# Kernel tuning notes

Hardware: AMD Instinct MI355X
Metric: run time of the kernel (lower is better)

Reference implementation:

```python
import jax, jax.numpy as jnp
import numpy as np
import math

S, B, E, H = 4096, 2, 1024, 16
D = E // H  # 64, projection dim used for scaling
LN_EPS = 1e-5

def setup_inputs() -> dict:
    key = jax.random.key(0)
    ks = jax.random.split(key, 3)
    std = 1.0 / math.sqrt(E)
    return {
        "src_emb": jax.random.normal(ks[0], (S, B, E), dtype=jnp.float32),
        "gamma": jnp.ones((E,), dtype=jnp.float32),
        "beta": jnp.zeros((E,), dtype=jnp.float32),
        "Wq": jax.random.normal(ks[1], (E, D), dtype=jnp.float32) * std,
        "bq": jnp.zeros((D,), dtype=jnp.float32),
        "Wk": jax.random.normal(ks[2], (E, D), dtype=jnp.float32) * std,
        "bk": jnp.zeros((D,), dtype=jnp.float32),
    }

def reference(src_emb, gamma, beta, Wq, bq, Wk, bk):
    # [S, B, E] -> [B, S, E]
    x = jnp.swapaxes(src_emb, 0, 1)
    # LayerNorm over last dim
    mu = jnp.mean(x, axis=-1, keepdims=True)
    var = jnp.mean(jnp.square(x - mu), axis=-1, keepdims=True)
    x = (x - mu) * jax.lax.rsqrt(var + LN_EPS) * gamma + beta
    # Q/K projections to head dim D
    q = x @ Wq + bq  # [B, S, D]
    k = x @ Wk + bk  # [B, S, D]
    scale = 1.0 / math.sqrt(D)
    # scaled bmm: [B, S(t), S(s)]
    scores = jnp.einsum("btd,bsd->bts", q * scale, k)
    # unnormalized softmax: row-max subtract then exp
    scores = scores - jnp.max(scores, axis=-1, keepdims=True)
    return jnp.exp(scores)
```

## Files before the change

kernel.cpp:

```cpp
#include <hip/hip_runtime.h>
#include <math.h>


typedef __attribute__((ext_vector_type(4))) float f32x4;
typedef __attribute__((ext_vector_type(8))) short bf16x8;
typedef __attribute__((ext_vector_type(8))) unsigned short u16x8;

#define SLEN 4096
#define BATCH 2
#define EDIM 1024
#define DDIM 64
#define KCH 256
#define XS_STRIDE 260
#define QK_STRIDE 136

__device__ __forceinline__ unsigned short f2bf(float f) {
    unsigned int u = __float_as_uint(f);
    u += 0x7FFFu + ((u >> 16) & 1u);
    return (unsigned short)(u >> 16);
}
__device__ __forceinline__ float bf2f(unsigned short h) {
    return __uint_as_float(((unsigned int)h) << 16);
}

__global__ __launch_bounds__(256) void wprep_kernel(
    const float* __restrict__ Wq, const float* __restrict__ Wk,
    unsigned short* __restrict__ whf, unsigned short* __restrict__ wlf)
{
    const int slot = blockIdx.x * 256 + threadIdx.x;
    const int ct = slot >> 11;
    const int kg = (slot >> 6) & 31;
    const int l  = slot & 63;
    const int c  = ct * 16 + (l & 15);
    const int kb = kg * 32 + ((l >> 4) & 3) * 8;
    const float* Wm = (c < DDIM) ? (Wq + c) : (Wk + (c - DDIM));
    u16x8 hv, lv;
#pragma unroll
    for (int j = 0; j < 8; ++j) {
        const float v = Wm[(size_t)(kb + j) * DDIM];
        const unsigned short h = f2bf(v);
        hv[j] = h;
        lv[j] = f2bf(v - bf2f(h));
    }
    *reinterpret_cast<u16x8*>(whf + (size_t)slot * 8) = hv;
    *reinterpret_cast<u16x8*>(wlf + (size_t)slot * 8) = lv;
}

__global__ __launch_bounds__(256, 2) void ln_proj_kernel(
    const float* __restrict__ src, const float* __restrict__ gamma,
    const float* __restrict__ beta,
    const float* __restrict__ bq, const float* __restrict__ bk,
    const unsigned short* __restrict__ whf, const unsigned short* __restrict__ wlf,
    unsigned short* __restrict__ qhf, unsigned short* __restrict__ qlf,
    unsigned short* __restrict__ khf, unsigned short* __restrict__ klf)
{
    __shared__ float xs[2][16][XS_STRIDE];
    __shared__ float2 stats[16];
    const int tid  = threadIdx.x;
    const int lane = tid & 63;
    const int wv   = tid >> 6;
    const int bid  = blockIdx.x;
    const int b    = bid >> 8;
    const int s0   = (bid & 255) * 16;

    for (int ii = 0; ii < 4; ++ii) {
        const int i = wv * 4 + ii;
        const float* row = src + ((size_t)(s0 + i) * BATCH + b) * EDIM;
        float sum = 0.f, sq = 0.f;
#pragma unroll
        for (int k = 0; k < 4; ++k) {
            float4 v = *reinterpret_cast<const float4*>(row + k * 256 + lane * 4);
            sum += v.x + v.y + v.z + v.w;
            sq  += v.x*v.x + v.y*v.y + v.z*v.z + v.w*v.w;
        }
#pragma unroll
        for (int off = 1; off < 64; off <<= 1) {
            sum += __shfl_xor(sum, off);
            sq  += __shfl_xor(sq,  off);
        }
        if (lane == 0) {
            const float mu   = sum * (1.f / EDIM);
            const float rstd = rsqrtf(sq * (1.f / EDIM) - mu * mu + 1e-5f);
            stats[i] = make_float2(mu, rstd);
        }
    }
    __syncthreads();

    const int srow = tid >> 4;
    const int se   = (tid & 15) * 4;
    const float* srcrow = src + ((size_t)(s0 + srow) * BATCH + b) * EDIM;
    const float smu = stats[srow].x;
    const float srs = stats[srow].y;

    const int ct0 = wv * 2;
    const int arow = lane & 15;
    const int koff = (lane >> 4) * 8;
    f32x4 acc0 = {0.f, 0.f, 0.f, 0.f};
    f32x4 acc1 = {0.f, 0.f, 0.f, 0.f};

#pragma unroll
    for (int t = 0; t < 4; ++t) {
        const int e = se + t * 64;
        float4 v  = *reinterpret_cast<const float4*>(srcrow + e);
        float4 g  = *reinterpret_cast<const float4*>(gamma + e);
        float4 bt = *reinterpret_cast<const float4*>(beta + e);
        float4 o;
        o.x = (v.x - smu) * srs * g.x + bt.x;
        o.y = (v.y - smu) * srs * g.y + bt.y;
        o.z = (v.z - smu) * srs * g.z + bt.z;
        o.w = (v.w - smu) * srs * g.w + bt.w;
        *reinterpret_cast<float4*>(&xs[0][srow][e]) = o;
    }
    __syncthreads();

    for (int c = 0; c < 4; ++c) {
        const int cur = c & 1;
        if (c < 3) {
            const int k0 = (c + 1) * KCH;
#pragma unroll
            for (int t = 0; t < 4; ++t) {
                const int e = se + t * 64;
                float4 v  = *reinterpret_cast<const float4*>(srcrow + k0 + e);
                float4 g  = *reinterpret_cast<const float4*>(gamma + k0 + e);
                float4 bt = *reinterpret_cast<const float4*>(beta + k0 + e);
                float4 o;
                o.x = (v.x - smu) * srs * g.x + bt.x;
                o.y = (v.y - smu) * srs * g.y + bt.y;
                o.z = (v.z - smu) * srs * g.z + bt.z;
                o.w = (v.w - smu) * srs * g.w + bt.w;
                *reinterpret_cast<float4*>(&xs[cur ^ 1][srow][e]) = o;
            }
        }
#pragma unroll 2
        for (int ks = 0; ks < 8; ++ks) {
            const int kg = c * 8 + ks;
            const float* xp = &xs[cur][arow][ks * 32 + koff];
            const float4 v0 = *reinterpret_cast<const float4*>(xp);
            const float4 v1 = *reinterpret_cast<const float4*>(xp + 4);
            const float vv[8] = {v0.x, v0.y, v0.z, v0.w, v1.x, v1.y, v1.z, v1.w};
            bf16x8 ah, al;
#pragma unroll
            for (int j = 0; j < 8; ++j) {
                const unsigned short h = f2bf(vv[j]);
                ah[j] = (short)h;
                al[j] = (short)f2bf(vv[j] - bf2f(h));
            }
            const size_t wb0 = ((size_t)(ct0 * 32 + kg) * 64 + lane) * 8;
            const size_t wb1 = wb0 + (size_t)32 * 64 * 8;
            const bf16x8 bh0 = *reinterpret_cast<const bf16x8*>(whf + wb0);
            const bf16x8 bl0 = *reinterpret_cast<const bf16x8*>(wlf + wb0);
            const bf16x8 bh1 = *reinterpret_cast<const bf16x8*>(whf + wb1);
            const bf16x8 bl1 = *reinterpret_cast<const bf16x8*>(wlf + wb1);
            acc0 = __builtin_amdgcn_mfma_f32_16x16x32_bf16(ah, bh0, acc0, 0, 0, 0);
            acc0 = __builtin_amdgcn_mfma_f32_16x16x32_bf16(al, bh0, acc0, 0, 0, 0);
            acc0 = __builtin_amdgcn_mfma_f32_16x16x32_bf16(ah, bl0, acc0, 0, 0, 0);
            acc0 = __builtin_amdgcn_mfma_f32_16x16x32_bf16(al, bl0, acc0, 0, 0, 0);
            acc1 = __builtin_amdgcn_mfma_f32_16x16x32_bf16(ah, bh1, acc1, 0, 0, 0);
            acc1 = __builtin_amdgcn_mfma_f32_16x16x32_bf16(al, bh1, acc1, 0, 0, 0);
            acc1 = __builtin_amdgcn_mfma_f32_16x16x32_bf16(ah, bl1, acc1, 0, 0, 0);
            acc1 = __builtin_amdgcn_mfma_f32_16x16x32_bf16(al, bl1, acc1, 0, 0, 0);
        }
        __syncthreads();
    }

    float* qk = &xs[0][0][0];
    {
        const int cj0 = ct0 * 16 + (lane & 15);
        const int cj1 = cj0 + 16;
        const int r0  = (lane >> 4) * 4;
        const float bv0 = (cj0 < DDIM) ? bq[cj0] : bk[cj0 - DDIM];
        const float bv1 = (cj1 < DDIM) ? bq[cj1] : bk[cj1 - DDIM];
        const int cb0 = (cj0 < DDIM) ? cj0 : (68 + cj0 - DDIM);
        const int cb1 = (cj1 < DDIM) ? cj1 : (68 + cj1 - DDIM);
#pragma unroll
        for (int r = 0; r < 4; ++r) {
            qk[(r0 + r) * QK_STRIDE + cb0] = acc0[r] + bv0;
            qk[(r0 + r) * QK_STRIDE + cb1] = acc1[r] + bv1;
        }
    }
    __syncthreads();

    {
        const int l2  = tid & 63;
        const int dc  = (tid >> 6) & 1;
        const int isK = tid >> 7;
        const int row = l2 & 15;
        const int d0  = dc * 32 + ((l2 >> 4) & 3) * 8;
        const float* p = &qk[row * QK_STRIDE + (isK ? 68 : 0) + d0];
        const float sc = isK ? 1.0f : 0.125f;
        u16x8 hvv, lvv;
#pragma unroll
        for (int j = 0; j < 8; ++j) {
            const float vq = p[j] * sc;
            const unsigned short h = f2bf(vq);
            hvv[j] = h;
            lvv[j] = f2bf(vq - bf2f(h));
        }
        const size_t base = ((((size_t)b * 256 + (size_t)(bid & 255)) * 2 + dc) * 512) + (size_t)l2 * 8;
        *reinterpret_cast<u16x8*>((isK ? khf : qhf) + base) = hvv;
        *reinterpret_cast<u16x8*>((isK ? klf : qlf) + base) = lvv;
    }
}

__global__ __launch_bounds__(1024, 1) void score_kernel(
    const unsigned short* __restrict__ qhf, const unsigned short* __restrict__ qlf,
    const unsigned short* __restrict__ khf, const unsigned short* __restrict__ klf,
    float* __restrict__ out)
{
    __shared__ float wmax[16 * 16];
    __shared__ float fmax_s[16];
    const int tid = threadIdx.x;
    const int l   = tid & 63;
    const int w   = tid >> 6;
    const int bid = blockIdx.x;
    const int b   = bid >> 8;
    const int rt  = bid & 255;

    const size_t abase = (((size_t)b * 256 + rt) * 2) * 512 + (size_t)l * 8;
    const bf16x8 qh0 = *reinterpret_cast<const bf16x8*>(qhf + abase);
    const bf16x8 qh1 = *reinterpret_cast<const bf16x8*>(qhf + abase + 512);
    const bf16x8 ql0 = *reinterpret_cast<const bf16x8*>(qlf + abase);
    const bf16x8 ql1 = *reinterpret_cast<const bf16x8*>(qlf + abase + 512);

    f32x4 acc[16];
#pragma unroll
    for (int i = 0; i < 16; ++i) acc[i] = (f32x4){0.f, 0.f, 0.f, 0.f};

#pragma unroll
    for (int i = 0; i < 16; ++i) {
        const int ct = w * 16 + i;
        const size_t kb = (((size_t)b * 256 + ct) * 2) * 512 + (size_t)l * 8;
        const bf16x8 kh0 = *reinterpret_cast<const bf16x8*>(khf + kb);
        const bf16x8 kh1 = *reinterpret_cast<const bf16x8*>(khf + kb + 512);
        const bf16x8 kl0 = *reinterpret_cast<const bf16x8*>(klf + kb);
        const bf16x8 kl1 = *reinterpret_cast<const bf16x8*>(klf + kb + 512);
        f32x4 a = acc[i];
        a = __builtin_amdgcn_mfma_f32_16x16x32_bf16(qh0, kh0, a, 0, 0, 0);
        a = __builtin_amdgcn_mfma_f32_16x16x32_bf16(qh1, kh1, a, 0, 0, 0);
        a = __builtin_amdgcn_mfma_f32_16x16x32_bf16(qh0, kl0, a, 0, 0, 0);
        a = __builtin_amdgcn_mfma_f32_16x16x32_bf16(qh1, kl1, a, 0, 0, 0);
        a = __builtin_amdgcn_mfma_f32_16x16x32_bf16(ql0, kh0, a, 0, 0, 0);
        a = __builtin_amdgcn_mfma_f32_16x16x32_bf16(ql1, kh1, a, 0, 0, 0);
        acc[i] = a;
    }

    float m4[4];
#pragma unroll
    for (int r = 0; r < 4; ++r) {
        m4[r] = acc[0][r];
#pragma unroll
        for (int i = 1; i < 16; ++i) m4[r] = fmaxf(m4[r], acc[i][r]);
    }
#pragma unroll
    for (int off = 1; off < 16; off <<= 1) {
#pragma unroll
        for (int r = 0; r < 4; ++r) m4[r] = fmaxf(m4[r], __shfl_xor(m4[r], off));
    }
    const int rgrp = l >> 4;
    if ((l & 15) == 0) {
#pragma unroll
        for (int r = 0; r < 4; ++r) wmax[w * 16 + rgrp * 4 + r] = m4[r];
    }
    __syncthreads();
    if (tid < 16) {
        float m = wmax[tid];
#pragma unroll
        for (int ww = 1; ww < 16; ++ww) m = fmaxf(m, wmax[ww * 16 + tid]);
        fmax_s[tid] = m;
    }
    __syncthreads();

    float fm[4];
#pragma unroll
    for (int r = 0; r < 4; ++r) fm[r] = fmax_s[rgrp * 4 + r];
    const int cres = l & 15;
    const size_t obase = ((size_t)b * SLEN + (size_t)rt * 16) * SLEN;
#pragma unroll
    for (int i = 0; i < 16; ++i) {
        const int col = (w * 16 + i) * 16 + cres;
#pragma unroll
        for (int r = 0; r < 4; ++r)
            out[obase + (size_t)(rgrp * 4 + r) * SLEN + col] = __expf(acc[i][r] - fm[r]);
    }
}

extern "C" void kernel_launch(void* const* d_in, const int* in_sizes, int n_in,
                              void* d_out, int out_size, void* d_ws, size_t ws_size,
                              hipStream_t stream) {
    (void)in_sizes; (void)n_in;
    const float* src   = (const float*)d_in[0];
    const float* gamma = (const float*)d_in[1];
    const float* beta  = (const float*)d_in[2];
    const float* Wq    = (const float*)d_in[3];
    const float* bq    = (const float*)d_in[4];
    const float* Wk    = (const float*)d_in[5];
    const float* bk    = (const float*)d_in[6];
    float* out = (float*)d_out;

    unsigned short* ws  = (unsigned short*)d_ws;
    unsigned short* qhf = ws;
    unsigned short* qlf = ws + (1u << 19);
    unsigned short* khf = ws + (2u << 19);
    unsigned short* klf = ws + (3u << 19);

    const size_t wfrag_shorts = 131072;
    const size_t need_bytes = (4u << 20) + 2 * 256 * 1024;
    unsigned short *whf, *wlf;
    if (ws_size >= need_bytes) {
        whf = ws + (4u << 19);
        wlf = whf + wfrag_shorts;
    } else {
        const size_t out_bytes = (size_t)out_size * 4;
        char* tail = (char*)d_out + (out_bytes - (2 * 256 * 1024 + 4096));
        whf = (unsigned short*)tail;
        wlf = whf + wfrag_shorts;
    }

    hipLaunchKernelGGL(wprep_kernel, dim3(64), dim3(256), 0, stream,
                       Wq, Wk, whf, wlf);
    hipLaunchKernelGGL(ln_proj_kernel, dim3(512), dim3(256), 0, stream,
                       src, gamma, beta, bq, bk, whf, wlf, qhf, qlf, khf, klf);
    hipLaunchKernelGGL(score_kernel, dim3(512), dim3(1024), 0, stream,
                       qhf, qlf, khf, klf, out);
}
```

Before: 75.08 us.

## Split fused LayerNorm-projection into LN, split-K MFMA projection, and reduce kernels

Replaces the single fused LayerNorm-plus-projection kernel with three kernels. The first normalizes rows and writes bf16 hi/lo fragments to global memory. The second runs a split-K MFMA projection over 1024 blocks, each covering two row tiles and one K quarter, writing partial sums. The third reduces the partials, adds bias and packs the Q/K fragments. The aim is more parallelism and MFMA reuse of weight fragments across two row tiles, at the cost of extra launches and a global round trip for the normalized activations and partial sums.

New measurement: 84.93 us. +13.1%, slower.

```diff
diff --git a/kernel.cpp b/kernel.cpp
--- a/kernel.cpp
+++ b/kernel.cpp
@@ -10,8 +10,6 @@
 #define BATCH 2
 #define EDIM 1024
 #define DDIM 64
-#define KCH 256
-#define XS_STRIDE 260
 #define QK_STRIDE 136
 
 __device__ __forceinline__ unsigned short f2bf(float f) {
@@ -46,22 +44,18 @@
     *reinterpret_cast<u16x8*>(wlf + (size_t)slot * 8) = lv;
 }
 
-__global__ __launch_bounds__(256, 2) void ln_proj_kernel(
+__global__ __launch_bounds__(256, 2) void ln_split_kernel(
     const float* __restrict__ src, const float* __restrict__ gamma,
     const float* __restrict__ beta,
-    const float* __restrict__ bq, const float* __restrict__ bk,
-    const unsigned short* __restrict__ whf, const unsigned short* __restrict__ wlf,
-    unsigned short* __restrict__ qhf, unsigned short* __restrict__ qlf,
-    unsigned short* __restrict__ khf, unsigned short* __restrict__ klf)
-{
-    __shared__ float xs[2][16][XS_STRIDE];
+    unsigned short* __restrict__ xh, unsigned short* __restrict__ xl)
+{
     __shared__ float2 stats[16];
     const int tid  = threadIdx.x;
     const int lane = tid & 63;
     const int wv   = tid >> 6;
-    const int bid  = blockIdx.x;
-    const int b    = bid >> 8;
-    const int s0   = (bid & 255) * 16;
+    const int gt   = blockIdx.x;
+    const int b    = gt >> 8;
+    const int s0   = (gt & 255) * 16;
 
     for (int ii = 0; ii < 4; ++ii) {
         const int i = wv * 4 + ii;
@@ -86,97 +80,129 @@
     }
     __syncthreads();
 
-    const int srow = tid >> 4;
-    const int se   = (tid & 15) * 4;
-    const float* srcrow = src + ((size_t)(s0 + srow) * BATCH + b) * EDIM;
-    const float smu = stats[srow].x;
-    const float srs = stats[srow].y;
-
-    const int ct0 = wv * 2;
-    const int arow = lane & 15;
-    const int koff = (lane >> 4) * 8;
+    const int row = lane & 15;
+    const int k4  = ((lane >> 4) & 3) * 8;
+    const float* srow = src + ((size_t)(s0 + row) * BATCH + b) * EDIM;
+    const float mu   = stats[row].x;
+    const float rstd = stats[row].y;
+#pragma unroll
+    for (int i = 0; i < 8; ++i) {
+        const int kg = wv * 8 + i;
+        const int kb = kg * 32 + k4;
+        const float4 va = *reinterpret_cast<const float4*>(srow + kb);
+        const float4 vb = *reinterpret_cast<const float4*>(srow + kb + 4);
+        const float4 ga = *reinterpret_cast<const float4*>(gamma + kb);
+        const float4 gb = *reinterpret_cast<const float4*>(gamma + kb + 4);
+        const float4 ba = *reinterpret_cast<const float4*>(beta + kb);
+        const float4 bb = *reinterpret_cast<const float4*>(beta + kb + 4);
+        const float vv[8] = {
+            (va.x - mu) * rstd * ga.x + ba.x, (va.y - mu) * rstd * ga.y + ba.y,
+            (va.z - mu) * rstd * ga.z + ba.z, (va.w - mu) * rstd * ga.w + ba.w,
+            (vb.x - mu) * rstd * gb.x + bb.x, (vb.y - mu) * rstd * gb.y + bb.y,
+            (vb.z - mu) * rstd * gb.z + bb.z, (vb.w - mu) * rstd * gb.w + bb.w };
+        u16x8 hv, lv;
+#pragma unroll
+        for (int j = 0; j < 8; ++j) {
+            const unsigned short h = f2bf(vv[j]);
+            hv[j] = h;
+            lv[j] = f2bf(vv[j] - bf2f(h));
+        }
+        const size_t slot = ((size_t)gt * 32 + kg) * 64 + lane;
+        *reinterpret_cast<u16x8*>(xh + slot * 8) = hv;
+        *reinterpret_cast<u16x8*>(xl + slot * 8) = lv;
+    }
+}
+
+__global__ __launch_bounds__(512, 4) void proj_kernel(
+    const unsigned short* __restrict__ xh, const unsigned short* __restrict__ xl,
+    const unsigned short* __restrict__ whf, const unsigned short* __restrict__ wlf,
+    float* __restrict__ pc)
+{
+    __shared__ u16x8 sa[2][2][8][64];
+    const int tid  = threadIdx.x;
+    const int lane = tid & 63;
+    const int ct   = tid >> 6;
+    const int bid  = blockIdx.x;
+    const int mg   = bid >> 2;
+    const int ksl  = bid & 3;
+    const int gt0  = mg * 2;
+
+    u16x8* sl = &sa[0][0][0][0];
+#pragma unroll
+    for (int p = 0; p < 4; ++p) {
+        const int sidx = p * 512 + tid;
+        const int hl   = sidx >> 10;
+        const int rem  = sidx & 1023;
+        const int t2   = rem >> 9;
+        const int kg   = (rem >> 6) & 7;
+        const int ln   = rem & 63;
+        const size_t gslot = (((size_t)(gt0 + t2)) * 32 + ksl * 8 + kg) * 64 + ln;
+        const unsigned short* srcp = hl ? xl : xh;
+        sl[sidx] = *reinterpret_cast<const u16x8*>(srcp + gslot * 8);
+    }
+    __syncthreads();
+
     f32x4 acc0 = {0.f, 0.f, 0.f, 0.f};
     f32x4 acc1 = {0.f, 0.f, 0.f, 0.f};
-
-#pragma unroll
-    for (int t = 0; t < 4; ++t) {
-        const int e = se + t * 64;
-        float4 v  = *reinterpret_cast<const float4*>(srcrow + e);
-        float4 g  = *reinterpret_cast<const float4*>(gamma + e);
-        float4 bt = *reinterpret_cast<const float4*>(beta + e);
-        float4 o;
-        o.x = (v.x - smu) * srs * g.x + bt.x;
-        o.y = (v.y - smu) * srs * g.y + bt.y;
-        o.z = (v.z - smu) * srs * g.z + bt.z;
-        o.w = (v.w - smu) * srs * g.w + bt.w;
-        *reinterpret_cast<float4*>(&xs[0][srow][e]) = o;
-    }
-    __syncthreads();
-
-    for (int c = 0; c < 4; ++c) {
-        const int cur = c & 1;
-        if (c < 3) {
-            const int k0 = (c + 1) * KCH;
-#pragma unroll
-            for (int t = 0; t < 4; ++t) {
-                const int e = se + t * 64;
-                float4 v  = *reinterpret_cast<const float4*>(srcrow + k0 + e);
-                float4 g  = *reinterpret_cast<const float4*>(gamma + k0 + e);
-                float4 bt = *reinterpret_cast<const float4*>(beta + k0 + e);
-                float4 o;
-                o.x = (v.x - smu) * srs * g.x + bt.x;
-                o.y = (v.y - smu) * srs * g.y + bt.y;
-                o.z = (v.z - smu) * srs * g.z + bt.z;
-                o.w = (v.w - smu) * srs * g.w + bt.w;
-                *reinterpret_cast<float4*>(&xs[cur ^ 1][srow][e]) = o;
-            }
-        }
-#pragma unroll 2
-        for (int ks = 0; ks < 8; ++ks) {
-            const int kg = c * 8 + ks;
-            const float* xp = &xs[cur][arow][ks * 32 + koff];
-            const float4 v0 = *reinterpret_cast<const float4*>(xp);
-            const float4 v1 = *reinterpret_cast<const float4*>(xp + 4);
-            const float vv[8] = {v0.x, v0.y, v0.z, v0.w, v1.x, v1.y, v1.z, v1.w};
-            bf16x8 ah, al;
-#pragma unroll
-            for (int j = 0; j < 8; ++j) {
-                const unsigned short h = f2bf(vv[j]);
-                ah[j] = (short)h;
-                al[j] = (short)f2bf(vv[j] - bf2f(h));
-            }
-            const size_t wb0 = ((size_t)(ct0 * 32 + kg) * 64 + lane) * 8;
-            const size_t wb1 = wb0 + (size_t)32 * 64 * 8;
-            const bf16x8 bh0 = *reinterpret_cast<const bf16x8*>(whf + wb0);
-            const bf16x8 bl0 = *reinterpret_cast<const bf16x8*>(wlf + wb0);
-            const bf16x8 bh1 = *reinterpret_cast<const bf16x8*>(whf + wb1);
-            const bf16x8 bl1 = *reinterpret_cast<const bf16x8*>(wlf + wb1);
-            acc0 = __builtin_amdgcn_mfma_f32_16x16x32_bf16(ah, bh0, acc0, 0, 0, 0);
-            acc0 = __builtin_amdgcn_mfma_f32_16x16x32_bf16(al, bh0, acc0, 0, 0, 0);
-            acc0 = __builtin_amdgcn_mfma_f32_16x16x32_bf16(ah, bl0, acc0, 0, 0, 0);
-            acc0 = __builtin_amdgcn_mfma_f32_16x16x32_bf16(al, bl0, acc0, 0, 0, 0);
-            acc1 = __builtin_amdgcn_mfma_f32_16x16x32_bf16(ah, bh1, acc1, 0, 0, 0);
-            acc1 = __builtin_amdgcn_mfma_f32_16x16x32_bf16(al, bh1, acc1, 0, 0, 0);
-            acc1 = __builtin_amdgcn_mfma_f32_16x16x32_bf16(ah, bl1, acc1, 0, 0, 0);
-            acc1 = __builtin_amdgcn_mfma_f32_16x16x32_bf16(al, bl1, acc1, 0, 0, 0);
-        }
-        __syncthreads();
-    }
-
-    float* qk = &xs[0][0][0];
+#pragma unroll
+    for (int kg = 0; kg < 8; ++kg) {
+        const bf16x8 ah0 = *reinterpret_cast<const bf16x8*>(&sa[0][0][kg][lane]);
+        const bf16x8 al0 = *reinterpret_cast<const bf16x8*>(&sa[1][0][kg][lane]);
+        const bf16x8 ah1 = *reinterpret_cast<const bf16x8*>(&sa[0][1][kg][lane]);
+        const bf16x8 al1 = *reinterpret_cast<const bf16x8*>(&sa[1][1][kg][lane]);
+        const size_t wslot = ((size_t)ct * 32 + ksl * 8 + kg) * 64 + lane;
+        const bf16x8 bh = *reinterpret_cast<const bf16x8*>(whf + wslot * 8);
+        const bf16x8 bl = *reinterpret_cast<const bf16x8*>(wlf + wslot * 8);
+        acc0 = __builtin_amdgcn_mfma_f32_16x16x32_bf16(ah0, bh, acc0, 0, 0, 0);
+        acc1 = __builtin_amdgcn_mfma_f32_16x16x32_bf16(ah1, bh, acc1, 0, 0, 0);
+        acc0 = __builtin_amdgcn_mfma_f32_16x16x32_bf16(al0, bh, acc0, 0, 0, 0);
+        acc1 = __builtin_amdgcn_mfma_f32_16x16x32_bf16(al1, bh, acc1, 0, 0, 0);
+        acc0 = __builtin_amdgcn_mfma_f32_16x16x32_bf16(ah0, bl, acc0, 0, 0, 0);
+        acc1 = __builtin_amdgcn_mfma_f32_16x16x32_bf16(ah1, bl, acc1, 0, 0, 0);
+        acc0 = __builtin_amdgcn_mfma_f32_16x16x32_bf16(al0, bl, acc0, 0, 0, 0);
+        acc1 = __builtin_amdgcn_mfma_f32_16x16x32_bf16(al1, bl, acc1, 0, 0, 0);
+    }
     {
-        const int cj0 = ct0 * 16 + (lane & 15);
-        const int cj1 = cj0 + 16;
-        const int r0  = (lane >> 4) * 4;
-        const float bv0 = (cj0 < DDIM) ? bq[cj0] : bk[cj0 - DDIM];
-        const float bv1 = (cj1 < DDIM) ? bq[cj1] : bk[cj1 - DDIM];
-        const int cb0 = (cj0 < DDIM) ? cj0 : (68 + cj0 - DDIM);
-        const int cb1 = (cj1 < DDIM) ? cj1 : (68 + cj1 - DDIM);
-#pragma unroll
-        for (int r = 0; r < 4; ++r) {
-            qk[(r0 + r) * QK_STRIDE + cb0] = acc0[r] + bv0;
-            qk[(r0 + r) * QK_STRIDE + cb1] = acc1[r] + bv1;
-        }
+        const size_t p0 = ((((size_t)gt0 * 4) + ksl) * 8 + ct) * 64 + lane;
+        const size_t p1 = ((((size_t)(gt0 + 1) * 4) + ksl) * 8 + ct) * 64 + lane;
+        float4 o0 = {acc0[0], acc0[1], acc0[2], acc0[3]};
+        float4 o1 = {acc1[0], acc1[1], acc1[2], acc1[3]};
+        *reinterpret_cast<float4*>(pc + p0 * 4) = o0;
+        *reinterpret_cast<float4*>(pc + p1 * 4) = o1;
+    }
+}
+
+__global__ __launch_bounds__(256, 2) void reduce_kernel(
+    const float* __restrict__ pc,
+    const float* __restrict__ bq, const float* __restrict__ bk,
+    unsigned short* __restrict__ qhf, unsigned short* __restrict__ qlf,
+    unsigned short* __restrict__ khf, unsigned short* __restrict__ klf)
+{
+    __shared__ float qk[16 * QK_STRIDE];
+    const int tid  = threadIdx.x;
+    const int lane = tid & 63;
+    const int wv   = tid >> 6;
+    const int gt   = blockIdx.x;
+    const int b    = gt >> 8;
+
+#pragma unroll
+    for (int cti = 0; cti < 2; ++cti) {
+        const int ct = wv * 2 + cti;
+        float4 s = {0.f, 0.f, 0.f, 0.f};
+#pragma unroll
+        for (int ksl = 0; ksl < 4; ++ksl) {
+            const size_t p = ((((size_t)gt * 4) + ksl) * 8 + ct) * 64 + lane;
+            const float4 v = *reinterpret_cast<const float4*>(pc + p * 4);
+            s.x += v.x; s.y += v.y; s.z += v.z; s.w += v.w;
+        }
+        const int cj = ct * 16 + (lane & 15);
+        const int r0 = (lane >> 4) * 4;
+        const float bv = (cj < DDIM) ? bq[cj] : bk[cj - DDIM];
+        const int cb = (cj < DDIM) ? cj : (68 + cj - DDIM);
+        qk[(r0 + 0) * QK_STRIDE + cb] = s.x + bv;
+        qk[(r0 + 1) * QK_STRIDE + cb] = s.y + bv;
+        qk[(r0 + 2) * QK_STRIDE + cb] = s.z + bv;
+        qk[(r0 + 3) * QK_STRIDE + cb] = s.w + bv;
     }
     __syncthreads();
 
@@ -196,7 +222,7 @@
             hvv[j] = h;
             lvv[j] = f2bf(vq - bf2f(h));
         }
-        const size_t base = ((((size_t)b * 256 + (size_t)(bid & 255)) * 2 + dc) * 512) + (size_t)l2 * 8;
+        const size_t base = ((((size_t)b * 256 + (size_t)(gt & 255)) * 2 + dc) * 512) + (size_t)l2 * 8;
         *reinterpret_cast<u16x8*>((isK ? khf : qhf) + base) = hvv;
         *reinterpret_cast<u16x8*>((isK ? klf : qlf) + base) = lvv;
     }
@@ -303,23 +329,37 @@
     unsigned short* khf = ws + (2u << 19);
     unsigned short* klf = ws + (3u << 19);
 
-    const size_t wfrag_shorts = 131072;
-    const size_t need_bytes = (4u << 20) + 2 * 256 * 1024;
-    unsigned short *whf, *wlf;
-    if (ws_size >= need_bytes) {
+    const size_t WF = 131072;
+    const size_t XF = 8388608;
+    const size_t big_bytes = 2 * WF * 2 + 2 * XF * 2 + (size_t)4194304 * 4;
+    const size_t need = (4u << 20) + big_bytes;
+    unsigned short *whf, *wlf, *xh, *xl;
+    float* pc;
+    if (ws_size >= need) {
         whf = ws + (4u << 19);
-        wlf = whf + wfrag_shorts;
+        wlf = whf + WF;
+        xh  = wlf + WF;
+        xl  = xh + XF;
+        pc  = (float*)(xl + XF);
     } else {
         const size_t out_bytes = (size_t)out_size * 4;
-        char* tail = (char*)d_out + (out_bytes - (2 * 256 * 1024 + 4096));
-        whf = (unsigned short*)tail;
-        wlf = whf + wfrag_shorts;
+        size_t base = (out_bytes - big_bytes) & ~(size_t)255;
+        char* tp = (char*)d_out + base;
+        whf = (unsigned short*)tp;            tp += WF * 2;
+        wlf = (unsigned short*)tp;            tp += WF * 2;
+        xh  = (unsigned short*)tp;            tp += XF * 2;
+        xl  = (unsigned short*)tp;            tp += XF * 2;
+        pc  = (float*)tp;
     }
 
     hipLaunchKernelGGL(wprep_kernel, dim3(64), dim3(256), 0, stream,
                        Wq, Wk, whf, wlf);
-    hipLaunchKernelGGL(ln_proj_kernel, dim3(512), dim3(256), 0, stream,
-                       src, gamma, beta, bq, bk, whf, wlf, qhf, qlf, khf, klf);
+    hipLaunchKernelGGL(ln_split_kernel, dim3(512), dim3(256), 0, stream,
+                       src, gamma, beta, xh, xl);
+    hipLaunchKernelGGL(proj_kernel, dim3(1024), dim3(512), 0, stream,
+                       xh, xl, whf, wlf, pc);
+    hipLaunchKernelGGL(reduce_kernel, dim3(512), dim3(256), 0, stream,
+                       pc, bq, bk, qhf, qlf, khf, klf);
     hipLaunchKernelGGL(score_kernel, dim3(512), dim3(1024), 0, stream,
                        qhf, qlf, khf, klf, out);
 }
```

## Split LN-projection across 8 waves and stage bf16 hi/lo splits in LDS once

Applied to the files above, without the earlier changes.

The LayerNorm+QK projection kernel now launches 512 threads per block, with each of eight waves computing one 16-column output tile instead of four waves computing two. Normalized activations are converted to bf16 hi/lo pairs once while staging and stored in MFMA fragment layout in LDS, so the per-k-step conversion repeated for each output tile goes away. The change is meant to shorten the serial MFMA chain per wave and cut redundant conversion work. In exchange, blocks are larger and add more LDS traffic and synchronisation. This kernel is a small part of the total, since the score kernel dominates.

Result: faster. 73.37 us (-2.3%).

```diff
diff --git a/kernel.cpp b/kernel.cpp
--- a/kernel.cpp
+++ b/kernel.cpp
@@ -10,8 +10,6 @@
 #define BATCH 2
 #define EDIM 1024
 #define DDIM 64
-#define KCH 256
-#define XS_STRIDE 260
 #define QK_STRIDE 136
 
 __device__ __forceinline__ unsigned short f2bf(float f) {
@@ -46,7 +44,7 @@
     *reinterpret_cast<u16x8*>(wlf + (size_t)slot * 8) = lv;
 }
 
-__global__ __launch_bounds__(256, 2) void ln_proj_kernel(
+__global__ __launch_bounds__(512, 2) void ln_proj_kernel(
     const float* __restrict__ src, const float* __restrict__ gamma,
     const float* __restrict__ beta,
     const float* __restrict__ bq, const float* __restrict__ bk,
@@ -54,17 +52,19 @@
     unsigned short* __restrict__ qhf, unsigned short* __restrict__ qlf,
     unsigned short* __restrict__ khf, unsigned short* __restrict__ klf)
 {
-    __shared__ float xs[2][16][XS_STRIDE];
+    __shared__ u16x8 xhf[2][8][64];
+    __shared__ u16x8 xlf[2][8][64];
     __shared__ float2 stats[16];
+    __shared__ float qk[16 * QK_STRIDE];
     const int tid  = threadIdx.x;
     const int lane = tid & 63;
     const int wv   = tid >> 6;
-    const int bid  = blockIdx.x;
-    const int b    = bid >> 8;
-    const int s0   = (bid & 255) * 16;
-
-    for (int ii = 0; ii < 4; ++ii) {
-        const int i = wv * 4 + ii;
+    const int gt   = blockIdx.x;
+    const int b    = gt >> 8;
+    const int s0   = (gt & 255) * 16;
+
+    for (int ii = 0; ii < 2; ++ii) {
+        const int i = wv * 2 + ii;
         const float* row = src + ((size_t)(s0 + i) * BATCH + b) * EDIM;
         float sum = 0.f, sq = 0.f;
 #pragma unroll
@@ -86,101 +86,73 @@
     }
     __syncthreads();
 
-    const int srow = tid >> 4;
-    const int se   = (tid & 15) * 4;
+    const int srow = lane & 15;
+    const int scol = wv * 32 + (lane >> 4) * 8;
     const float* srcrow = src + ((size_t)(s0 + srow) * BATCH + b) * EDIM;
     const float smu = stats[srow].x;
     const float srs = stats[srow].y;
 
-    const int ct0 = wv * 2;
-    const int arow = lane & 15;
-    const int koff = (lane >> 4) * 8;
-    f32x4 acc0 = {0.f, 0.f, 0.f, 0.f};
-    f32x4 acc1 = {0.f, 0.f, 0.f, 0.f};
-
-#pragma unroll
-    for (int t = 0; t < 4; ++t) {
-        const int e = se + t * 64;
-        float4 v  = *reinterpret_cast<const float4*>(srcrow + e);
-        float4 g  = *reinterpret_cast<const float4*>(gamma + e);
-        float4 bt = *reinterpret_cast<const float4*>(beta + e);
-        float4 o;
-        o.x = (v.x - smu) * srs * g.x + bt.x;
-        o.y = (v.y - smu) * srs * g.y + bt.y;
-        o.z = (v.z - smu) * srs * g.z + bt.z;
-        o.w = (v.w - smu) * srs * g.w + bt.w;
-        *reinterpret_cast<float4*>(&xs[0][srow][e]) = o;
-    }
+#define STAGE(c, bf)                                                          \
+    {                                                                         \
+        const int cb_ = (c) * 256 + scol;                                     \
+        const float4 va = *reinterpret_cast<const float4*>(srcrow + cb_);     \
+        const float4 vb = *reinterpret_cast<const float4*>(srcrow + cb_ + 4); \
+        const float4 ga = *reinterpret_cast<const float4*>(gamma + cb_);      \
+        const float4 gb = *reinterpret_cast<const float4*>(gamma + cb_ + 4);  \
+        const float4 ba = *reinterpret_cast<const float4*>(beta + cb_);       \
+        const float4 bb = *reinterpret_cast<const float4*>(beta + cb_ + 4);   \
+        const float vv[8] = {                                                 \
+            (va.x - smu) * srs * ga.x + ba.x, (va.y - smu) * srs * ga.y + ba.y,\
+            (va.z - smu) * srs * ga.z + ba.z, (va.w - smu) * srs * ga.w + ba.w,\
+            (vb.x - smu) * srs * gb.x + bb.x, (vb.y - smu) * srs * gb.y + bb.y,\
+            (vb.z - smu) * srs * gb.z + bb.z, (vb.w - smu) * srs * gb.w + bb.w };\
+        u16x8 hv, lv;                                                         \
+        _Pragma("unroll")                                                     \
+        for (int j = 0; j < 8; ++j) {                                         \
+            const unsigned short h = f2bf(vv[j]);                             \
+            hv[j] = h;                                                        \
+            lv[j] = f2bf(vv[j] - bf2f(h));                                    \
+        }                                                                     \
+        xhf[bf][wv][lane] = hv;                                               \
+        xlf[bf][wv][lane] = lv;                                               \
+    }
+
+    f32x4 acc = {0.f, 0.f, 0.f, 0.f};
+
+    STAGE(0, 0);
     __syncthreads();
 
     for (int c = 0; c < 4; ++c) {
         const int cur = c & 1;
-        if (c < 3) {
-            const int k0 = (c + 1) * KCH;
-#pragma unroll
-            for (int t = 0; t < 4; ++t) {
-                const int e = se + t * 64;
-                float4 v  = *reinterpret_cast<const float4*>(srcrow + k0 + e);
-                float4 g  = *reinterpret_cast<const float4*>(gamma + k0 + e);
-                float4 bt = *reinterpret_cast<const float4*>(beta + k0 + e);
-                float4 o;
-                o.x = (v.x - smu) * srs * g.x + bt.x;
-                o.y = (v.y - smu) * srs * g.y + bt.y;
-                o.z = (v.z - smu) * srs * g.z + bt.z;
-                o.w = (v.w - smu) * srs * g.w + bt.w;
-                *reinterpret_cast<float4*>(&xs[cur ^ 1][srow][e]) = o;
-            }
-        }
-#pragma unroll 2
-        for (int ks = 0; ks < 8; ++ks) {
-            const int kg = c * 8 + ks;
-            const float* xp = &xs[cur][arow][ks * 32 + koff];
-            const float4 v0 = *reinterpret_cast<const float4*>(xp);
-            const float4 v1 = *reinterpret_cast<const float4*>(xp + 4);
-            const float vv[8] = {v0.x, v0.y, v0.z, v0.w, v1.x, v1.y, v1.z, v1.w};
-            bf16x8 ah, al;
-#pragma unroll
-            for (int j = 0; j < 8; ++j) {
-                const unsigned short h = f2bf(vv[j]);
-                ah[j] = (short)h;
-                al[j] = (short)f2bf(vv[j] - bf2f(h));
-            }
-            const size_t wb0 = ((size_t)(ct0 * 32 + kg) * 64 + lane) * 8;
-            const size_t wb1 = wb0 + (size_t)32 * 64 * 8;
-            const bf16x8 bh0 = *reinterpret_cast<const bf16x8*>(whf + wb0);
-            const bf16x8 bl0 = *reinterpret_cast<const bf16x8*>(wlf + wb0);
-            const bf16x8 bh1 = *reinterpret_cast<const bf16x8*>(whf + wb1);
-            const bf16x8 bl1 = *reinterpret_cast<const bf16x8*>(wlf + wb1);
-            acc0 = __builtin_amdgcn_mfma_f32_16x16x32_bf16(ah, bh0, acc0, 0, 0, 0);
-            acc0 = __builtin_amdgcn_mfma_f32_16x16x32_bf16(al, bh0, acc0, 0, 0, 0);
-            acc0 = __builtin_amdgcn_mfma_f32_16x16x32_bf16(ah, bl0, acc0, 0, 0, 0);
-            acc0 = __builtin_amdgcn_mfma_f32_16x16x32_bf16(al, bl0, acc0, 0, 0, 0);
-            acc1 = __builtin_amdgcn_mfma_f32_16x16x32_bf16(ah, bh1, acc1, 0, 0, 0);
-            acc1 = __builtin_amdgcn_mfma_f32_16x16x32_bf16(al, bh1, acc1, 0, 0, 0);
-            acc1 = __builtin_amdgcn_mfma_f32_16x16x32_bf16(ah, bl1, acc1, 0, 0, 0);
-            acc1 = __builtin_amdgcn_mfma_f32_16x16x32_bf16(al, bl1, acc1, 0, 0, 0);
+        if (c < 3) STAGE(c + 1, cur ^ 1);
+#pragma unroll
+        for (int kg = 0; kg < 8; ++kg) {
+            const bf16x8 ah = *reinterpret_cast<const bf16x8*>(&xhf[cur][kg][lane]);
+            const bf16x8 al = *reinterpret_cast<const bf16x8*>(&xlf[cur][kg][lane]);
+            const size_t wslot = ((size_t)wv * 32 + c * 8 + kg) * 64 + lane;
+            const bf16x8 bh = *reinterpret_cast<const bf16x8*>(whf + wslot * 8);
+            const bf16x8 bl = *reinterpret_cast<const bf16x8*>(wlf + wslot * 8);
+            acc = __builtin_amdgcn_mfma_f32_16x16x32_bf16(ah, bh, acc, 0, 0, 0);
+            acc = __builtin_amdgcn_mfma_f32_16x16x32_bf16(al, bh, acc, 0, 0, 0);
+            acc = __builtin_amdgcn_mfma_f32_16x16x32_bf16(ah, bl, acc, 0, 0, 0);
+            acc = __builtin_amdgcn_mfma_f32_16x16x32_bf16(al, bl, acc, 0, 0, 0);
         }
         __syncthreads();
     }
-
-    float* qk = &xs[0][0][0];
+#undef STAGE
+
     {
-        const int cj0 = ct0 * 16 + (lane & 15);
-        const int cj1 = cj0 + 16;
-        const int r0  = (lane >> 4) * 4;
-        const float bv0 = (cj0 < DDIM) ? bq[cj0] : bk[cj0 - DDIM];
-        const float bv1 = (cj1 < DDIM) ? bq[cj1] : bk[cj1 - DDIM];
-        const int cb0 = (cj0 < DDIM) ? cj0 : (68 + cj0 - DDIM);
-        const int cb1 = (cj1 < DDIM) ? cj1 : (68 + cj1 - DDIM);
-#pragma unroll
-        for (int r = 0; r < 4; ++r) {
-            qk[(r0 + r) * QK_STRIDE + cb0] = acc0[r] + bv0;
-            qk[(r0 + r) * QK_STRIDE + cb1] = acc1[r] + bv1;
-        }
-    }
-    __syncthreads();
-
-    {
+        const int cj = wv * 16 + (lane & 15);
+        const int r0 = (lane >> 4) * 4;
+        const float bv = (cj < DDIM) ? bq[cj] : bk[cj - DDIM];
+        const int cb = (cj < DDIM) ? cj : (68 + cj - DDIM);
+#pragma unroll
+        for (int r = 0; r < 4; ++r)
+            qk[(r0 + r) * QK_STRIDE + cb] = acc[r] + bv;
+    }
+    __syncthreads();
+
+    if (tid < 256) {
         const int l2  = tid & 63;
         const int dc  = (tid >> 6) & 1;
         const int isK = tid >> 7;
@@ -196,7 +168,7 @@
             hvv[j] = h;
             lvv[j] = f2bf(vq - bf2f(h));
         }
-        const size_t base = ((((size_t)b * 256 + (size_t)(bid & 255)) * 2 + dc) * 512) + (size_t)l2 * 8;
+        const size_t base = ((((size_t)b * 256 + (size_t)(gt & 255)) * 2 + dc) * 512) + (size_t)l2 * 8;
         *reinterpret_cast<u16x8*>((isK ? khf : qhf) + base) = hvv;
         *reinterpret_cast<u16x8*>((isK ? klf : qlf) + base) = lvv;
     }
@@ -318,7 +290,7 @@
 
     hipLaunchKernelGGL(wprep_kernel, dim3(64), dim3(256), 0, stream,
                        Wq, Wk, whf, wlf);
-    hipLaunchKernelGGL(ln_proj_kernel, dim3(512), dim3(256), 0, stream,
+    hipLaunchKernelGGL(ln_proj_kernel, dim3(512), dim3(512), 0, stream,
                        src, gamma, beta, bq, bk, whf, wlf, qhf, qlf, khf, klf);
     hipLaunchKernelGGL(score_kernel, dim3(512), dim3(1024), 0, stream,
                        qhf, qlf, khf, klf, out);
```
